# Optimization experiments

Hardware: AMD Instinct MI355X
Metric: run time of the kernel (lower is better)

## Reference

```python
import jax, jax.numpy as jnp
import numpy as np

T_TRACK = 256   # tracklets per graph
M_DET = 256     # detections per graph
N_NODES = T_TRACK + M_DET
D_IN = 512      # raw node feature dim (stand-in for CNN crop features)
D_EMB = 256     # node embedding dim
SLACK = 0.2
LAM = 5.0
SINK_ITERS = 8


def box_iou(a, b):
    # a, b: [E,4] boxes (x1,y1,x2,y2)
    ix1 = jnp.maximum(a[:, 0], b[:, 0])
    iy1 = jnp.maximum(a[:, 1], b[:, 1])
    ix2 = jnp.minimum(a[:, 2], b[:, 2])
    iy2 = jnp.minimum(a[:, 3], b[:, 3])
    inter = jnp.clip(ix2 - ix1, 0.0) * jnp.clip(iy2 - iy1, 0.0)
    area_a = (a[:, 2] - a[:, 0]) * (a[:, 3] - a[:, 1])
    area_b = (b[:, 2] - b[:, 0]) * (b[:, 3] - b[:, 1])
    return inter / (area_a + area_b - inter + 1e-8)


def mlp2(x, W1, b1, W2, b2):
    return jax.nn.sigmoid(jax.nn.relu(x @ W1 + b1) @ W2 + b2)


def setup_inputs() -> dict:
    key = jax.random.key(0)
    ks = jax.random.split(key, 16)
    x = jax.random.normal(ks[0], (N_NODES, D_IN), jnp.float32)
    coords = jax.random.uniform(ks[1], (N_NODES, 4), jnp.float32)
    # valid boxes: x1<x2, y1<y2
    c = jax.random.uniform(ks[2], (N_NODES, 2), jnp.float32) * 100.0
    wh = jax.random.uniform(ks[3], (N_NODES, 2), jnp.float32) * 20.0 + 1.0
    coords_original = jnp.concatenate([c, c + wh], axis=1)
    # bipartite edges: track i (node i) <-> det j (node T_TRACK+j), both directions;
    # first T*M edges satisfy src < dst (the half kept by the row<col mask)
    src = jnp.repeat(jnp.arange(T_TRACK, dtype=jnp.int32), M_DET)
    dst = jnp.tile(jnp.arange(M_DET, dtype=jnp.int32) + T_TRACK, T_TRACK)
    edge_index = jnp.stack([jnp.concatenate([src, dst]), jnp.concatenate([dst, src])])
    s = 0.05
    p = lambda k, shp: jax.random.normal(k, shp, jnp.float32) * s
    return dict(
        x=x, coords=coords, coords_original=coords_original, edge_index=edge_index,
        W_cnn=p(ks[4], (D_IN, D_EMB)), b_cnn=jnp.zeros((D_EMB,), jnp.float32),
        Wapp1=p(ks[5], (2 * D_EMB, 128)), bapp1=jnp.zeros((128,), jnp.float32),
        Wapp2=p(ks[6], (128, 1)), bapp2=jnp.zeros((1,), jnp.float32),
        Wg1=p(ks[7], (8, 32)), bg1=jnp.zeros((32,), jnp.float32),
        Wg2=p(ks[8], (32, 1)), bg2=jnp.zeros((1,), jnp.float32),
        Wa1=p(ks[9], (2, 8)), ba1=jnp.zeros((8,), jnp.float32),
        Wa2=p(ks[10], (8, 1)), ba2=jnp.zeros((1,), jnp.float32),
        Wo1=p(ks[11], (D_EMB, D_EMB)), Wo2=p(ks[12], (D_EMB, D_EMB)),
        bo=jnp.zeros((D_EMB,), jnp.float32),
        Wf1=p(ks[13], (2, 8)), bf1=jnp.zeros((8,), jnp.float32),
        Wf2=p(ks[14], (8, 1)), bf2=jnp.zeros((1,), jnp.float32),
    )


def reference(x, coords, coords_original, edge_index, W_cnn, b_cnn, Wapp1, bapp1, Wapp2, bapp2, Wg1, bg1, Wg2, bg2, Wa1, ba1, Wa2, ba2, Wo1, Wo2, bo, Wf1, bf1, Wf2, bf2):
    src, dst = edge_index[0], edge_index[1]
    h = jax.nn.relu(x @ W_cnn + b_cnn)                      # [N, D]
    # per-edge appearance / geometry affinities (vectorized over all edges)
    app = mlp2(jnp.concatenate([h[src], h[dst]], 1), Wapp1, bapp1, Wapp2, bapp2)[:, 0]
    geo = mlp2(jnp.concatenate([coords[src], coords[dst]], 1), Wg1, bg1, Wg2, bg2)[:, 0]
    iou = box_iou(coords_original[src], coords_original[dst])
    e = mlp2(jnp.stack([app, geo], -1), Wa1, ba1, Wa2, ba2)[:, 0]   # [E]
    # message passing (optimNet): edge-gated neighbor aggregation
    agg = jax.ops.segment_sum(e[:, None] * h[src], dst, num_segments=N_NODES)
    out = jax.nn.relu(h @ Wo1 + agg @ Wo2 + bo)             # [N, D]
    # directed (src < dst) half of the edges only
    eh = T_TRACK * M_DET
    a, b = out[src[:eh]], out[dst[:eh]]
    na = jnp.maximum(jnp.linalg.norm(a, axis=-1), 1e-6)
    nb = jnp.maximum(jnp.linalg.norm(b, axis=-1), 1e-6)
    cos = jnp.sum(a * b, -1) / (na * nb)
    score = mlp2(jnp.stack([cos, iou[:eh]], -1), Wf1, bf1, Wf2, bf2)[:, 0]
    # assignment matrix with slack row/col, Sinkhorn normalization
    slack_v = jnp.exp(jnp.float32(LAM * SLACK))
    mat = jnp.full((T_TRACK + 1, M_DET + 1), slack_v, jnp.float32)
    mat = mat.at[:T_TRACK, :M_DET].set(jnp.exp(LAM * score).reshape(T_TRACK, M_DET))
    for _ in range(SINK_ITERS):
        mat = mat / jnp.sum(mat, axis=1, keepdims=True)
        mat = mat / jnp.sum(mat, axis=0, keepdims=True)
    return mat[:T_TRACK, :M_DET].reshape(-1)                # [T*M]
```

## Files before the change

kernel.cpp:

```cpp
#include <hip/hip_runtime.h>
#include <math.h>


__device__ __forceinline__ float sigmoidf_(float x) { return 1.0f / (1.0f + expf(-x)); }

typedef _Float16 h2t __attribute__((ext_vector_type(2)));

__device__ __forceinline__ h2t pack2(float x, float y) {
  h2t r; r.x = (_Float16)x; r.y = (_Float16)y; return r;
}
__device__ __forceinline__ float fdot2f(h2t a, h2t b, float c) {
  return __builtin_amdgcn_fdot2(a, b, c, false);
}
template <int CTRL>
__device__ __forceinline__ float dpp_get(float x) {
  return __builtin_bit_cast(
      float, __builtin_amdgcn_mov_dpp(__builtin_bit_cast(int, x), CTRL, 0xF, 0xF, false));
}
template <int IMM>
__device__ __forceinline__ float swz_get(float x) {
  return __builtin_bit_cast(
      float, __builtin_amdgcn_ds_swizzle(__builtin_bit_cast(int, x), IMM));
}
__device__ __forceinline__ float allred16(float x) {
  x += dpp_get<0xB1>(x);
  x += dpp_get<0x4E>(x);
  x += dpp_get<0x141>(x);
  x += dpp_get<0x140>(x);
  return x;
}

#define G_LOAD(T, AREG, BARR, AP, BP, LDB)                             \
  {                                                                    \
    AREG = *reinterpret_cast<const float4*>((AP) + (T) * 32);          \
    _Pragma("unroll") for (int kk = 0; kk < 32; ++kk)                  \
        BARR[kk] = (BP)[((T) * 32 + kk) * (LDB)];                      \
  }
#define G_STORE(BUF, AREG)                                             \
  {                                                                    \
    Ast[BUF][ac + 0][ar] = AREG.x; Ast[BUF][ac + 1][ar] = AREG.y;      \
    Ast[BUF][ac + 2][ar] = AREG.z; Ast[BUF][ac + 3][ar] = AREG.w;      \
  }
#define G_COMP(BUF, BARR)                                              \
  {                                                                    \
    _Pragma("unroll") for (int kk = 0; kk < 32; ++kk) {                \
      const float4 a4 =                                                \
          *reinterpret_cast<const float4*>(&Ast[BUF][kk][4 * ty]);     \
      const float bv = BARR[kk];                                       \
      acc[0] = fmaf(a4.x, bv, acc[0]); acc[1] = fmaf(a4.y, bv, acc[1]);\
      acc[2] = fmaf(a4.z, bv, acc[2]); acc[3] = fmaf(a4.w, bv, acc[3]);\
    }                                                                  \
  }

__global__ __launch_bounds__(256)
void k1_h(const float* __restrict__ x, const float* __restrict__ Wc,
          const float* __restrict__ bc, float* __restrict__ h) {
  __shared__ __align__(16) float Ast[2][32][36];
  const int tid = threadIdx.x;
  const int tx = tid & 31, ty = tid >> 5;
  const int ar = tid >> 3, ac = (tid & 7) * 4;
  const int bm = blockIdx.y * 32, bn = blockIdx.x * 32;
  const float* __restrict__ Bp = Wc + bn + tx;
  const float* __restrict__ Ap = x + (bm + ar) * 512 + ac;
  float4 aA, aB;
  float bA[32], bB[32];
  float acc[4] = {0.f, 0.f, 0.f, 0.f};

  G_LOAD(0, aA, bA, Ap, Bp, 256);
  G_STORE(0, aA);
  __syncthreads();
  for (int t = 0; t < 16; t += 2) {
    G_LOAD(t + 1, aB, bB, Ap, Bp, 256);
    G_COMP(0, bA);
    G_STORE(1, aB);
    __syncthreads();
    if (t + 2 < 16) { G_LOAD(t + 2, aA, bA, Ap, Bp, 256); }
    G_COMP(1, bB);
    if (t + 2 < 16) { G_STORE(0, aA); }
    __syncthreads();
  }
  const float bias = bc[bn + tx];
#pragma unroll
  for (int i = 0; i < 4; ++i) {
    const float vv = acc[i] + bias;
    h[(bm + 4 * ty + i) * 256 + bn + tx] = vv > 0.f ? vv : 0.f;
  }
}

__global__ __launch_bounds__(256)
void k2_pqgw(const float* __restrict__ h, const float* __restrict__ W1,
             const float* __restrict__ b1, const float* __restrict__ Wo2,
             const float* __restrict__ Wo1, float* __restrict__ PQGW) {
  __shared__ __align__(16) float Ast[2][32][36];
  const int tid = threadIdx.x;
  const int tx = tid & 31, ty = tid >> 5;
  const int ar = tid >> 3, ac = (tid & 7) * 4;
  const int bm = blockIdx.y * 32, bn = blockIdx.x * 32;
  const int col = bn + tx;
  const float* __restrict__ Bp;
  int ldb;
  if (bn < 128)       { Bp = W1 + col; ldb = 128; }
  else if (bn < 256)  { Bp = W1 + 256 * 128 + (col - 128); ldb = 128; }
  else if (bn < 512)  { Bp = Wo2 + (col - 256); ldb = 256; }
  else                { Bp = Wo1 + (col - 512); ldb = 256; }
  const float* __restrict__ Ap = h + (bm + ar) * 256 + ac;
  float4 aA, aB;
  float bA[32], bB[32];
  float acc[4] = {0.f, 0.f, 0.f, 0.f};

  G_LOAD(0, aA, bA, Ap, Bp, ldb);
  G_STORE(0, aA);
  __syncthreads();
  for (int t = 0; t < 8; t += 2) {
    G_LOAD(t + 1, aB, bB, Ap, Bp, ldb);
    G_COMP(0, bA);
    G_STORE(1, aB);
    __syncthreads();
    if (t + 2 < 8) { G_LOAD(t + 2, aA, bA, Ap, Bp, ldb); }
    G_COMP(1, bB);
    if (t + 2 < 8) { G_STORE(0, aA); }
    __syncthreads();
  }
  const float bias = (bn < 128) ? b1[col] : 0.f;
#pragma unroll
  for (int i = 0; i < 4; ++i)
    PQGW[(bm + 4 * ty + i) * 768 + col] = acc[i] + bias;
}

__global__ __launch_bounds__(256)
void k34_edges_out(const float* __restrict__ PQGW, const float* __restrict__ coords,
                   const float* __restrict__ co, const float* __restrict__ Wapp2,
                   const float* __restrict__ bapp2, const float* __restrict__ Wg1,
                   const float* __restrict__ bg1, const float* __restrict__ Wg2,
                   const float* __restrict__ bg2, const float* __restrict__ Wa1,
                   const float* __restrict__ ba1, const float* __restrict__ Wa2,
                   const float* __restrict__ ba2, const float* __restrict__ bo,
                   float* __restrict__ iou1, float* __restrict__ outm,
                   float* __restrict__ nrm) {
  __shared__ __align__(16) float sQ[128], sW2[128], sWg1[256], sWg2[32], sGfix[32];
  __shared__ __align__(16) float sE[256];
  __shared__ float sWa1[16], sBa1[8], sWa2[8], wpart[4];
  const int tid = threadIdx.x;
  const int b = blockIdx.x;
  const bool istrack = (b < 256);
  const int vbase = istrack ? 256 : 0;

  if (tid < 128) {
    sQ[tid] = PQGW[b * 768 + 128 + tid];
    sW2[tid] = Wapp2[tid];
  }
  sWg1[tid] = Wg1[tid];
  if (tid < 32) sWg2[tid] = Wg2[tid];
  if (tid < 16) sWa1[tid] = Wa1[tid];
  if (tid < 8) { sBa1[tid] = ba1[tid]; sWa2[tid] = Wa2[tid]; }
  __syncthreads();
  if (tid < 32) {
    float g = bg1[tid];
#pragma unroll
    for (int q = 0; q < 4; ++q)
      g = fmaf(coords[b * 4 + q], sWg1[(4 + q) * 32 + tid], g);
    sGfix[tid] = g;
  }
  __syncthreads();

  const int vr = vbase + tid;
  const float* prow = PQGW + vr * 768;
  float z = 0.f;
#pragma unroll
  for (int j = 0; j < 128; j += 4) {
    const float4 p4 = *reinterpret_cast<const float4*>(prow + j);
    const float4 q4 = *reinterpret_cast<const float4*>(&sQ[j]);
    const float4 w4 = *reinterpret_cast<const float4*>(&sW2[j]);
    float a;
    a = p4.x + q4.x; a = a > 0.f ? a : 0.f; z = fmaf(a, w4.x, z);
    a = p4.y + q4.y; a = a > 0.f ? a : 0.f; z = fmaf(a, w4.y, z);
    a = p4.z + q4.z; a = a > 0.f ? a : 0.f; z = fmaf(a, w4.z, z);
    a = p4.w + q4.w; a = a > 0.f ? a : 0.f; z = fmaf(a, w4.w, z);
  }
  const float app = sigmoidf_(z + bapp2[0]);
  const float4 cp = *reinterpret_cast<const float4*>(coords + vr * 4);
  float gz = 0.f;
#pragma unroll
  for (int m = 0; m < 32; ++m) {
    float hm = sGfix[m];
    hm = fmaf(cp.x, sWg1[0 * 32 + m], hm);
    hm = fmaf(cp.y, sWg1[1 * 32 + m], hm);
    hm = fmaf(cp.z, sWg1[2 * 32 + m], hm);
    hm = fmaf(cp.w, sWg1[3 * 32 + m], hm);
    hm = hm > 0.f ? hm : 0.f;
    gz = fmaf(hm, sWg2[m], gz);
  }
  const float geo = sigmoidf_(gz + bg2[0]);
  float ez = 0.f;
#pragma unroll
  for (int m = 0; m < 8; ++m) {
    float hm = fmaf(app, sWa1[m], fmaf(geo, sWa1[8 + m], sBa1[m]));
    hm = hm > 0.f ? hm : 0.f;
    ez = fmaf(hm, sWa2[m], ez);
  }
  sE[tid] = sigmoidf_(ez + ba2[0]);
  if (istrack) {
    const float4 A4 = *reinterpret_cast<const float4*>(co + b * 4);
    const float4 B4 = *reinterpret_cast<const float4*>(co + (256 + tid) * 4);
    const float ix1 = fmaxf(A4.x, B4.x), iy1 = fmaxf(A4.y, B4.y);
    const float ix2 = fminf(A4.z, B4.z), iy2 = fminf(A4.w, B4.w);
    const float inter = fmaxf(ix2 - ix1, 0.f) * fmaxf(iy2 - iy1, 0.f);
    const float areaA = (A4.z - A4.x) * (A4.w - A4.y);
    const float areaB = (B4.z - B4.x) * (B4.w - B4.y);
    iou1[b * 256 + tid] = inter / (areaA + areaB - inter + 1e-8f);
  }
  __syncthreads();

  const int c = tid;
  float a0 = 0.f, a1 = 0.f, a2 = 0.f, a3 = 0.f;
  const float* gcol = PQGW + vbase * 768 + 256 + c;
#pragma unroll 4
  for (int j = 0; j < 256; j += 4) {
    const float4 e4 = *reinterpret_cast<const float4*>(&sE[j]);
    a0 = fmaf(e4.x, gcol[(j + 0) * 768], a0);
    a1 = fmaf(e4.y, gcol[(j + 1) * 768], a1);
    a2 = fmaf(e4.z, gcol[(j + 2) * 768], a2);
    a3 = fmaf(e4.w, gcol[(j + 3) * 768], a3);
  }
  const float base = PQGW[b * 768 + 512 + c] + bo[c];
  float vv = base + ((a0 + a1) + (a2 + a3));
  vv = vv > 0.f ? vv : 0.f;
  outm[b * 256 + c] = vv;
  float nsq = vv * vv;
  nsq = allred16(nsq);
  nsq += swz_get<0x401F>(nsq);
  nsq += __shfl_xor(nsq, 32, 64);
  if ((tid & 63) == 0) wpart[tid >> 6] = nsq;
  __syncthreads();
  if (tid == 0)
    nrm[b] = fmaxf(sqrtf(wpart[0] + wpart[1] + wpart[2] + wpart[3]), 1e-6f);
}

__global__ __launch_bounds__(256)
void k6_score(const float* __restrict__ outm, const float* __restrict__ nrm,
              const float* __restrict__ iou1, const float* __restrict__ Wf1,
              const float* __restrict__ bf1, const float* __restrict__ Wf2,
              const float* __restrict__ bf2, float* __restrict__ Mblk) {
  __shared__ __align__(16) float Ast[2][32][36];
  const int tid = threadIdx.x;
  const int tx = tid & 31, ty = tid >> 5;
  const int ar = tid >> 3, ac = (tid & 7) * 4;
  const int s0 = blockIdx.y * 32, d0 = blockIdx.x * 32;
  const float* __restrict__ Ap = outm + (s0 + ar) * 256 + ac;
  const float* __restrict__ Bp = outm + (256 + d0 + tx) * 256;
  float4 aA, aB;
  float bA[32], bB[32];
  float acc[4] = {0.f, 0.f, 0.f, 0.f};

  G_LOAD(0, aA, bA, Ap, Bp, 1);
  G_STORE(0, aA);
  __syncthreads();
  for (int t = 0; t < 8; t += 2) {
    G_LOAD(t + 1, aB, bB, Ap, Bp, 1);
    G_COMP(0, bA);
    G_STORE(1, aB);
    __syncthreads();
    if (t + 2 < 8) { G_LOAD(t + 2, aA, bA, Ap, Bp, 1); }
    G_COMP(1, bB);
    if (t + 2 < 8) { G_STORE(0, aA); }
    __syncthreads();
  }
  const float nb = nrm[256 + d0 + tx];
  float w1c[8], w1i[8], w2[8];
#pragma unroll
  for (int m = 0; m < 8; ++m) {
    w1c[m] = Wf1[m]; w1i[m] = Wf1[8 + m]; w2[m] = Wf2[m];
  }
  const float bf20 = bf2[0];
#pragma unroll
  for (int i = 0; i < 4; ++i) {
    const int r = s0 + 4 * ty + i;
    const float cosv = acc[i] / (nrm[r] * nb);
    const float i1 = iou1[r * 256 + d0 + tx];
    float sz = 0.f;
#pragma unroll
    for (int m = 0; m < 8; ++m) {
      float hm = fmaf(cosv, w1c[m], fmaf(i1, w1i[m], bf1[m]));
      hm = hm > 0.f ? hm : 0.f;
      sz = fmaf(hm, w2[m], sz);
    }
    const float score = sigmoidf_(sz + bf20);
    Mblk[r * 256 + d0 + tx] = expf(5.0f * score);
  }
}

__global__ __launch_bounds__(1024)
void k7_sink(const float* __restrict__ Mg, float* __restrict__ outp) {
  __shared__ __align__(16) float su_f[256];
  __shared__ __align__(16) float svs_f[256];
  __shared__ __align__(16) float psum[16][260];
  __shared__ float wsumU[16], wsumV[4];
  const int tid = threadIdx.x, w = tid >> 6, l = tid & 63;
  const float slack = 2.71828182845904523536f;
  const float INV256 = 0.00390625f;
  const int rev = ((l & 1) << 3) | ((l & 2) << 1) | ((l & 4) >> 1) | ((l & 8) >> 3);
  const bool b0 = l & 1, b1 = l & 2, b2 = l & 4, b3 = l & 8;

  h2t mrA[16], mrB[16];
#pragma unroll
  for (int i = 0; i < 16; ++i) {
    const float4 f = *reinterpret_cast<const float4*>(Mg + (w * 16 + i) * 256 + 4 * l);
    mrA[i] = pack2(f.x, f.y);
    mrB[i] = pack2(f.z, f.w);
  }
  if (tid < 256) svs_f[tid] = 256.0f;
  __syncthreads();

  float sv256 = 1.0f;
  for (int it = 0; it < 8; ++it) {
    const float sv_tot =
        (it == 0) ? 257.0f : (wsumV[0] + wsumV[1] + wsumV[2] + wsumV[3] + sv256);
    const float su256 = 1.0f / (slack * sv_tot);
    const float4 va = *reinterpret_cast<const float4*>(&svs_f[4 * l]);
    const h2t sva = pack2(va.x, va.y), svb = pack2(va.z, va.w);
    float p[16];
#pragma unroll
    for (int i = 0; i < 16; ++i) p[i] = fdot2f(mrA[i], sva, fdot2f(mrB[i], svb, 0.0f));
#pragma unroll
    for (int i = 0; i < 8; ++i) {
      const float keep = b0 ? p[i + 8] : p[i], give = b0 ? p[i] : p[i + 8];
      p[i] = keep + dpp_get<0xB1>(give);
    }
#pragma unroll
    for (int i = 0; i < 4; ++i) {
      const float keep = b1 ? p[i + 4] : p[i], give = b1 ? p[i] : p[i + 4];
      p[i] = keep + dpp_get<0x4E>(give);
    }
#pragma unroll
    for (int i = 0; i < 2; ++i) {
      const float keep = b2 ? p[i + 2] : p[i], give = b2 ? p[i] : p[i + 2];
      p[i] = keep + dpp_get<0x141>(give);
    }
    {
      const float keep = b3 ? p[1] : p[0], give = b3 ? p[0] : p[1];
      p[0] = keep + dpp_get<0x140>(give);
    }
    float S = p[0];
    S += swz_get<0x401F>(S);
    S += __shfl_xor(S, 32, 64);
    const float su_val = 1.0f / (S * INV256 + slack * sv256);
    if (l < 16) su_f[w * 16 + rev] = su_val;
    const float wsU = allred16(su_val);
    if (l == 0) wsumU[w] = wsU;
    asm volatile("s_waitcnt lgkmcnt(0)" ::: "memory");
    float su16[16];
#pragma unroll
    for (int k = 0; k < 16; k += 4) {
      const float4 t = *reinterpret_cast<const float4*>(&su_f[w * 16 + k]);
      su16[k] = t.x; su16[k + 1] = t.y; su16[k + 2] = t.z; su16[k + 3] = t.w;
    }
    float pc0 = 0.f, pc1 = 0.f, pc2 = 0.f, pc3 = 0.f;
#pragma unroll
    for (int i = 0; i < 16; ++i) {
      const float ui = su16[i];
      pc0 = fmaf((float)mrA[i].x, ui, pc0);
      pc1 = fmaf((float)mrA[i].y, ui, pc1);
      pc2 = fmaf((float)mrB[i].x, ui, pc2);
      pc3 = fmaf((float)mrB[i].y, ui, pc3);
    }
    float4 pcv; pcv.x = pc0; pcv.y = pc1; pcv.z = pc2; pcv.w = pc3;
    *reinterpret_cast<float4*>(&psum[w][4 * l]) = pcv;
    __syncthreads();
    const float su_tot = wsumU[0] + wsumU[1] + wsumU[2] + wsumU[3] + wsumU[4] +
                         wsumU[5] + wsumU[6] + wsumU[7] + wsumU[8] + wsumU[9] +
                         wsumU[10] + wsumU[11] + wsumU[12] + wsumU[13] +
                         wsumU[14] + wsumU[15] + su256;
    if (tid < 256) {
      float cs = 0.f;
#pragma unroll
      for (int g = 0; g < 16; ++g) cs += psum[g][tid];
      const float sv_val = 1.0f / (cs + slack * su256);
      svs_f[tid] = 256.0f * sv_val;
      float t = allred16(sv_val);
      t += swz_get<0x401F>(t);
      t += __shfl_xor(t, 32, 64);
      if (l == 0) wsumV[w] = t;
    }
    sv256 = 1.0f / (slack * su_tot);
    __syncthreads();
  }
  const float4 sv4 = *reinterpret_cast<const float4*>(&svs_f[4 * l]);
#pragma unroll
  for (int i = 0; i < 16; ++i) {
    const float uo = su_f[w * 16 + i] * INV256;
    float4 o;
    o.x = uo * (float)mrA[i].x * sv4.x;
    o.y = uo * (float)mrA[i].y * sv4.y;
    o.z = uo * (float)mrB[i].x * sv4.z;
    o.w = uo * (float)mrB[i].y * sv4.w;
    *reinterpret_cast<float4*>(outp + (w * 16 + i) * 256 + 4 * l) = o;
  }
}

extern "C" void kernel_launch(void* const* d_in, const int* in_sizes, int n_in,
                              void* d_out, int out_size, void* d_ws, size_t ws_size,
                              hipStream_t stream) {
  (void)in_sizes; (void)n_in; (void)out_size; (void)ws_size;
  const float* x      = (const float*)d_in[0];
  const float* coords = (const float*)d_in[1];
  const float* co     = (const float*)d_in[2];
  const float* Wc    = (const float*)d_in[4];
  const float* bc    = (const float*)d_in[5];
  const float* Wapp1 = (const float*)d_in[6];
  const float* bapp1 = (const float*)d_in[7];
  const float* Wapp2 = (const float*)d_in[8];
  const float* bapp2 = (const float*)d_in[9];
  const float* Wg1   = (const float*)d_in[10];
  const float* bg1   = (const float*)d_in[11];
  const float* Wg2   = (const float*)d_in[12];
  const float* bg2   = (const float*)d_in[13];
  const float* Wa1   = (const float*)d_in[14];
  const float* ba1   = (const float*)d_in[15];
  const float* Wa2   = (const float*)d_in[16];
  const float* ba2   = (const float*)d_in[17];
  const float* Wo1   = (const float*)d_in[18];
  const float* Wo2   = (const float*)d_in[19];
  const float* bo    = (const float*)d_in[20];
  const float* Wf1   = (const float*)d_in[21];
  const float* bf1   = (const float*)d_in[22];
  const float* Wf2   = (const float*)d_in[23];
  const float* bf2   = (const float*)d_in[24];

  float* ws   = (float*)d_ws;
  float* h    = ws + 0;
  float* PQGW = ws + 131072;
  float* iou1 = ws + 524288;
  float* outm = ws + 589824;
  float* nrm  = ws + 720896;
  float* Mblk = ws + 721408;

  k1_h<<<dim3(8, 16), 256, 0, stream>>>(x, Wc, bc, h);
  k2_pqgw<<<dim3(24, 16), 256, 0, stream>>>(h, Wapp1, bapp1, Wo2, Wo1, PQGW);
  k34_edges_out<<<512, 256, 0, stream>>>(PQGW, coords, co, Wapp2, bapp2, Wg1,
                                         bg1, Wg2, bg2, Wa1, ba1, Wa2, ba2, bo,
                                         iou1, outm, nrm);
  k6_score<<<dim3(8, 8), 256, 0, stream>>>(outm, nrm, iou1, Wf1, bf1, Wf2, bf2,
                                           Mblk);
  k7_sink<<<1, 1024, 0, stream>>>(Mblk, (float*)d_out);
}
```

Baseline: 95.95 us.

## Split-K first GEMM, transpose P output, move IoU into score kernel

The first GEMM is split along K into two halves over a z grid dimension, doubling block count (128 to 256). The second GEMM sums the two partial results and applies bias and ReLU while loading A. The P projection is written transposed so the per-node appearance MLP in the edge kernel reads coalesced columns instead of strided rows. IoU computation moves from the edge kernel into the score kernel, removing the iou1 buffer round trip. This adds extra partial-sum traffic and A-side loads in the second GEMM.

```diff
diff --git a/kernel.cpp b/kernel.cpp
--- a/kernel.cpp
+++ b/kernel.cpp
@@ -54,14 +54,16 @@
 
 __global__ __launch_bounds__(256)
 void k1_h(const float* __restrict__ x, const float* __restrict__ Wc,
-          const float* __restrict__ bc, float* __restrict__ h) {
+          float* __restrict__ hAB) {
   __shared__ __align__(16) float Ast[2][32][36];
   const int tid = threadIdx.x;
   const int tx = tid & 31, ty = tid >> 5;
   const int ar = tid >> 3, ac = (tid & 7) * 4;
   const int bm = blockIdx.y * 32, bn = blockIdx.x * 32;
-  const float* __restrict__ Bp = Wc + bn + tx;
-  const float* __restrict__ Ap = x + (bm + ar) * 512 + ac;
+  const int z = blockIdx.z;
+  const float* __restrict__ Bp = Wc + (z * 256) * 256 + bn + tx;
+  const float* __restrict__ Ap = x + (bm + ar) * 512 + z * 256 + ac;
+  float* __restrict__ Cout = hAB + z * 131072;
   float4 aA, aB;
   float bA[32], bB[32];
   float acc[4] = {0.f, 0.f, 0.f, 0.f};
@@ -69,28 +71,26 @@
   G_LOAD(0, aA, bA, Ap, Bp, 256);
   G_STORE(0, aA);
   __syncthreads();
-  for (int t = 0; t < 16; t += 2) {
+  for (int t = 0; t < 8; t += 2) {
     G_LOAD(t + 1, aB, bB, Ap, Bp, 256);
     G_COMP(0, bA);
     G_STORE(1, aB);
     __syncthreads();
-    if (t + 2 < 16) { G_LOAD(t + 2, aA, bA, Ap, Bp, 256); }
+    if (t + 2 < 8) { G_LOAD(t + 2, aA, bA, Ap, Bp, 256); }
     G_COMP(1, bB);
-    if (t + 2 < 16) { G_STORE(0, aA); }
-    __syncthreads();
-  }
-  const float bias = bc[bn + tx];
-#pragma unroll
-  for (int i = 0; i < 4; ++i) {
-    const float vv = acc[i] + bias;
-    h[(bm + 4 * ty + i) * 256 + bn + tx] = vv > 0.f ? vv : 0.f;
-  }
+    if (t + 2 < 8) { G_STORE(0, aA); }
+    __syncthreads();
+  }
+#pragma unroll
+  for (int i = 0; i < 4; ++i)
+    Cout[(bm + 4 * ty + i) * 256 + bn + tx] = acc[i];
 }
 
 __global__ __launch_bounds__(256)
-void k2_pqgw(const float* __restrict__ h, const float* __restrict__ W1,
-             const float* __restrict__ b1, const float* __restrict__ Wo2,
-             const float* __restrict__ Wo1, float* __restrict__ PQGW) {
+void k2_pqgw(const float* __restrict__ hAB, const float* __restrict__ bc,
+             const float* __restrict__ W1, const float* __restrict__ b1,
+             const float* __restrict__ Wo2, const float* __restrict__ Wo1,
+             float* __restrict__ PQGW, float* __restrict__ PT) {
   __shared__ __align__(16) float Ast[2][32][36];
   const int tid = threadIdx.x;
   const int tx = tid & 31, ty = tid >> 5;
@@ -103,41 +103,63 @@
   else if (bn < 256)  { Bp = W1 + 256 * 128 + (col - 128); ldb = 128; }
   else if (bn < 512)  { Bp = Wo2 + (col - 256); ldb = 256; }
   else                { Bp = Wo1 + (col - 512); ldb = 256; }
-  const float* __restrict__ Ap = h + (bm + ar) * 256 + ac;
+  const float* __restrict__ ApA = hAB + (bm + ar) * 256 + ac;
+  const float* __restrict__ ApB = ApA + 131072;
+  const float* __restrict__ bcp = bc + ac;
   float4 aA, aB;
   float bA[32], bB[32];
   float acc[4] = {0.f, 0.f, 0.f, 0.f};
 
-  G_LOAD(0, aA, bA, Ap, Bp, ldb);
+#define K2_LOAD(T, AREG, BARR)                                         \
+  {                                                                    \
+    const float4 xa = *reinterpret_cast<const float4*>(ApA + (T) * 32);\
+    const float4 xb = *reinterpret_cast<const float4*>(ApB + (T) * 32);\
+    const float4 xc = *reinterpret_cast<const float4*>(bcp + (T) * 32);\
+    AREG.x = fmaxf(xa.x + xb.x + xc.x, 0.f);                           \
+    AREG.y = fmaxf(xa.y + xb.y + xc.y, 0.f);                           \
+    AREG.z = fmaxf(xa.z + xb.z + xc.z, 0.f);                           \
+    AREG.w = fmaxf(xa.w + xb.w + xc.w, 0.f);                           \
+    _Pragma("unroll") for (int kk = 0; kk < 32; ++kk)                  \
+        BARR[kk] = Bp[((T) * 32 + kk) * ldb];                          \
+  }
+
+  K2_LOAD(0, aA, bA);
   G_STORE(0, aA);
   __syncthreads();
   for (int t = 0; t < 8; t += 2) {
-    G_LOAD(t + 1, aB, bB, Ap, Bp, ldb);
+    K2_LOAD(t + 1, aB, bB);
     G_COMP(0, bA);
     G_STORE(1, aB);
     __syncthreads();
-    if (t + 2 < 8) { G_LOAD(t + 2, aA, bA, Ap, Bp, ldb); }
+    if (t + 2 < 8) { K2_LOAD(t + 2, aA, bA); }
     G_COMP(1, bB);
     if (t + 2 < 8) { G_STORE(0, aA); }
     __syncthreads();
   }
-  const float bias = (bn < 128) ? b1[col] : 0.f;
-#pragma unroll
-  for (int i = 0; i < 4; ++i)
-    PQGW[(bm + 4 * ty + i) * 768 + col] = acc[i] + bias;
+  if (bn < 128) {
+    const float bias = b1[col];
+#pragma unroll
+    for (int i = 0; i < 4; ++i)
+      PT[col * 512 + bm + 4 * ty + i] = acc[i] + bias;
+  } else {
+#pragma unroll
+    for (int i = 0; i < 4; ++i)
+      PQGW[(bm + 4 * ty + i) * 768 + col] = acc[i];
+  }
+#undef K2_LOAD
 }
 
 __global__ __launch_bounds__(256)
-void k34_edges_out(const float* __restrict__ PQGW, const float* __restrict__ coords,
-                   const float* __restrict__ co, const float* __restrict__ Wapp2,
+void k34_edges_out(const float* __restrict__ PQGW, const float* __restrict__ PT,
+                   const float* __restrict__ coords, const float* __restrict__ Wapp2,
                    const float* __restrict__ bapp2, const float* __restrict__ Wg1,
                    const float* __restrict__ bg1, const float* __restrict__ Wg2,
                    const float* __restrict__ bg2, const float* __restrict__ Wa1,
                    const float* __restrict__ ba1, const float* __restrict__ Wa2,
                    const float* __restrict__ ba2, const float* __restrict__ bo,
-                   float* __restrict__ iou1, float* __restrict__ outm,
-                   float* __restrict__ nrm) {
-  __shared__ __align__(16) float sQ[128], sW2[128], sWg1[256], sWg2[32], sGfix[32];
+                   float* __restrict__ outm, float* __restrict__ nrm) {
+  __shared__ __align__(16) float2 qw[128];
+  __shared__ __align__(16) float sWg1[256], sWg2[32], sGfix[32];
   __shared__ __align__(16) float sE[256];
   __shared__ float sWa1[16], sBa1[8], sWa2[8], wpart[4];
   const int tid = threadIdx.x;
@@ -146,8 +168,10 @@
   const int vbase = istrack ? 256 : 0;
 
   if (tid < 128) {
-    sQ[tid] = PQGW[b * 768 + 128 + tid];
-    sW2[tid] = Wapp2[tid];
+    float2 t2;
+    t2.x = PQGW[b * 768 + 128 + tid];
+    t2.y = Wapp2[tid];
+    qw[tid] = t2;
   }
   sWg1[tid] = Wg1[tid];
   if (tid < 32) sWg2[tid] = Wg2[tid];
@@ -164,18 +188,14 @@
   __syncthreads();
 
   const int vr = vbase + tid;
-  const float* prow = PQGW + vr * 768;
+  const float* __restrict__ ptb = PT + vr;
   float z = 0.f;
-#pragma unroll
-  for (int j = 0; j < 128; j += 4) {
-    const float4 p4 = *reinterpret_cast<const float4*>(prow + j);
-    const float4 q4 = *reinterpret_cast<const float4*>(&sQ[j]);
-    const float4 w4 = *reinterpret_cast<const float4*>(&sW2[j]);
-    float a;
-    a = p4.x + q4.x; a = a > 0.f ? a : 0.f; z = fmaf(a, w4.x, z);
-    a = p4.y + q4.y; a = a > 0.f ? a : 0.f; z = fmaf(a, w4.y, z);
-    a = p4.z + q4.z; a = a > 0.f ? a : 0.f; z = fmaf(a, w4.z, z);
-    a = p4.w + q4.w; a = a > 0.f ? a : 0.f; z = fmaf(a, w4.w, z);
+#pragma unroll 8
+  for (int j = 0; j < 128; ++j) {
+    const float2 q2 = qw[j];
+    float a = ptb[j * 512] + q2.x;
+    a = a > 0.f ? a : 0.f;
+    z = fmaf(a, q2.y, z);
   }
   const float app = sigmoidf_(z + bapp2[0]);
   const float4 cp = *reinterpret_cast<const float4*>(coords + vr * 4);
@@ -199,21 +219,11 @@
     ez = fmaf(hm, sWa2[m], ez);
   }
   sE[tid] = sigmoidf_(ez + ba2[0]);
-  if (istrack) {
-    const float4 A4 = *reinterpret_cast<const float4*>(co + b * 4);
-    const float4 B4 = *reinterpret_cast<const float4*>(co + (256 + tid) * 4);
-    const float ix1 = fmaxf(A4.x, B4.x), iy1 = fmaxf(A4.y, B4.y);
-    const float ix2 = fminf(A4.z, B4.z), iy2 = fminf(A4.w, B4.w);
-    const float inter = fmaxf(ix2 - ix1, 0.f) * fmaxf(iy2 - iy1, 0.f);
-    const float areaA = (A4.z - A4.x) * (A4.w - A4.y);
-    const float areaB = (B4.z - B4.x) * (B4.w - B4.y);
-    iou1[b * 256 + tid] = inter / (areaA + areaB - inter + 1e-8f);
-  }
   __syncthreads();
 
   const int c = tid;
   float a0 = 0.f, a1 = 0.f, a2 = 0.f, a3 = 0.f;
-  const float* gcol = PQGW + vbase * 768 + 256 + c;
+  const float* __restrict__ gcol = PQGW + vbase * 768 + 256 + c;
 #pragma unroll 4
   for (int j = 0; j < 256; j += 4) {
     const float4 e4 = *reinterpret_cast<const float4*>(&sE[j]);
@@ -238,7 +248,7 @@
 
 __global__ __launch_bounds__(256)
 void k6_score(const float* __restrict__ outm, const float* __restrict__ nrm,
-              const float* __restrict__ iou1, const float* __restrict__ Wf1,
+              const float* __restrict__ co, const float* __restrict__ Wf1,
               const float* __restrict__ bf1, const float* __restrict__ Wf2,
               const float* __restrict__ bf2, float* __restrict__ Mblk) {
   __shared__ __align__(16) float Ast[2][32][36];
@@ -266,6 +276,8 @@
     __syncthreads();
   }
   const float nb = nrm[256 + d0 + tx];
+  const float4 B4 = *reinterpret_cast<const float4*>(co + (256 + d0 + tx) * 4);
+  const float areaB = (B4.z - B4.x) * (B4.w - B4.y);
   float w1c[8], w1i[8], w2[8];
 #pragma unroll
   for (int m = 0; m < 8; ++m) {
@@ -275,8 +287,13 @@
 #pragma unroll
   for (int i = 0; i < 4; ++i) {
     const int r = s0 + 4 * ty + i;
+    const float4 A4 = *reinterpret_cast<const float4*>(co + r * 4);
+    const float ix1 = fmaxf(A4.x, B4.x), iy1 = fmaxf(A4.y, B4.y);
+    const float ix2 = fminf(A4.z, B4.z), iy2 = fminf(A4.w, B4.w);
+    const float inter = fmaxf(ix2 - ix1, 0.f) * fmaxf(iy2 - iy1, 0.f);
+    const float areaA = (A4.z - A4.x) * (A4.w - A4.y);
+    const float i1 = inter / (areaA + areaB - inter + 1e-8f);
     const float cosv = acc[i] / (nrm[r] * nb);
-    const float i1 = iou1[r * 256 + d0 + tx];
     float sz = 0.f;
 #pragma unroll
     for (int m = 0; m < 8; ++m) {
@@ -427,19 +444,20 @@
   const float* bf2   = (const float*)d_in[24];
 
   float* ws   = (float*)d_ws;
-  float* h    = ws + 0;
-  float* PQGW = ws + 131072;
-  float* iou1 = ws + 524288;
-  float* outm = ws + 589824;
-  float* nrm  = ws + 720896;
-  float* Mblk = ws + 721408;
-
-  k1_h<<<dim3(8, 16), 256, 0, stream>>>(x, Wc, bc, h);
-  k2_pqgw<<<dim3(24, 16), 256, 0, stream>>>(h, Wapp1, bapp1, Wo2, Wo1, PQGW);
-  k34_edges_out<<<512, 256, 0, stream>>>(PQGW, coords, co, Wapp2, bapp2, Wg1,
+  float* hAB  = ws + 0;
+  float* PQGW = ws + 262144;
+  float* PT   = ws + 655360;
+  float* outm = ws + 720896;
+  float* nrm  = ws + 851968;
+  float* Mblk = ws + 852480;
+
+  k1_h<<<dim3(8, 16, 2), 256, 0, stream>>>(x, Wc, hAB);
+  k2_pqgw<<<dim3(24, 16), 256, 0, stream>>>(hAB, bc, Wapp1, bapp1, Wo2, Wo1,
+                                            PQGW, PT);
+  k34_edges_out<<<512, 256, 0, stream>>>(PQGW, PT, coords, Wapp2, bapp2, Wg1,
                                          bg1, Wg2, bg2, Wa1, ba1, Wa2, ba2, bo,
-                                         iou1, outm, nrm);
-  k6_score<<<dim3(8, 8), 256, 0, stream>>>(outm, nrm, iou1, Wf1, bf1, Wf2, bf2,
+                                         outm, nrm);
+  k6_score<<<dim3(8, 8), 256, 0, stream>>>(outm, nrm, co, Wf1, bf1, Wf2, bf2,
                                            Mblk);
   k7_sink<<<1, 1024, 0, stream>>>(Mblk, (float*)d_out);
 }
```

Result: faster. 88.66 us (-7.6%).
